# Performance work log

Measured on AMD Instinct MI355X. Metric: run time of the kernel, lower is better.

## Reference

```python
import jax, jax.numpy as jnp
import numpy as np

B, L, D, H, W = 2, 2048, 1024, 16, 32
HD = D // H  # head_dim = 64


def setup_inputs() -> dict:
    key = jax.random.key(0)
    ks = jax.random.split(key, 9)
    x = jax.random.normal(ks[0], (B, L, D), dtype=jnp.float32)
    s = 1.0 / np.sqrt(D)
    wq = jax.random.normal(ks[1], (D, D), dtype=jnp.float32) * s
    wk = jax.random.normal(ks[2], (D, D), dtype=jnp.float32) * s
    wv = jax.random.normal(ks[3], (D, D), dtype=jnp.float32) * s
    wo = jax.random.normal(ks[4], (D, D), dtype=jnp.float32) * s
    # per-head SwiGLU connection nets: in_dim=1, hidden=128, out_dim=1
    cw1 = jax.random.normal(ks[5], (H, 128), dtype=jnp.float32) * 0.5
    cw2 = jax.random.normal(ks[6], (H, 128), dtype=jnp.float32) * (1.0 / np.sqrt(128))
    cw3 = jax.random.normal(ks[7], (H, 128), dtype=jnp.float32) * 0.5
    # rotary embedding tables (complex freqs_cis -> cos/sin), [L, HD//2]
    inv_freq = 1.0 / (10000.0 ** (np.arange(0, HD, 2, dtype=np.float32) / HD))
    t = np.arange(L, dtype=np.float32)
    ang = np.outer(t, inv_freq)
    rope_cos = jnp.asarray(np.cos(ang), dtype=jnp.float32)
    rope_sin = jnp.asarray(np.sin(ang), dtype=jnp.float32)
    return {"x": x, "wq": wq, "wk": wk, "wv": wv, "wo": wo,
            "cw1": cw1, "cw2": cw2, "cw3": cw3,
            "rope_cos": rope_cos, "rope_sin": rope_sin,
            "window_size": W}


def _rope(t, cos, sin):
    # t: [B,H,L,HD]; cos/sin: [L,HD//2] -> broadcast [1,1,L,HD//2]
    tr = t.reshape(*t.shape[:-1], -1, 2)
    t0, t1 = tr[..., 0], tr[..., 1]
    c = cos[None, None]
    s = sin[None, None]
    r0 = t0 * c - t1 * s
    r1 = t0 * s + t1 * c
    return jnp.stack([r0, r1], axis=-1).reshape(t.shape)


def reference(x, wq, wk, wv, wo, cw1, cw2, cw3, rope_cos, rope_sin, window_size):
    b, l, d = x.shape
    h = cw1.shape[0]
    hd = d // h
    w = window_size
    # projections (torch Linear: y = x W^T)
    Q = jnp.einsum('bld,ed->ble', x, wq).reshape(b, l, h, hd).transpose(0, 2, 1, 3)
    K = jnp.einsum('bld,ed->ble', x, wk).reshape(b, l, h, hd).transpose(0, 2, 1, 3)
    V = jnp.einsum('bld,ed->ble', x, wv).reshape(b, l, h, hd).transpose(0, 2, 1, 3)
    Q = _rope(Q, rope_cos, rope_sin)
    K = _rope(K, rope_cos, rope_sin)
    # causal sliding windows via zero left-padding (matches torch F.pad + unfold;
    # NOTE: padded zeros are NOT masked in softmax, faithfully reproduced)
    pad = w - 1
    Kp = jnp.pad(K, ((0, 0), (0, 0), (pad, 0), (0, 0)))
    Vp = jnp.pad(V, ((0, 0), (0, 0), (pad, 0), (0, 0)))
    idx = jnp.arange(l)[:, None] + jnp.arange(w)[None, :]  # [L,W] into padded axis
    Kw = Kp[:, :, idx, :]  # [B,H,L,W,HD]
    Vw = Vp[:, :, idx, :]
    scores = jnp.einsum('bhld,bhlwd->bhlw', Q, Kw) / jnp.sqrt(jnp.float32(hd))
    attn = jax.nn.softmax(scores, axis=-1)
    # per-head learned position weights: SwiGLU(pos) for pos in linspace(0,1,W)
    pos = jnp.linspace(0.0, 1.0, w)  # [W]
    a1 = pos[None, :, None] * cw1[:, None, :]   # [H,W,128]
    a3 = pos[None, :, None] * cw3[:, None, :]
    conn = jnp.einsum('hwk,hk->hw', jax.nn.silu(a1) * a3, cw2)  # [H,W]
    conn = jax.nn.softmax(conn, axis=-1)
    final = attn * conn[None, :, None, :]
    final = final / (final.sum(axis=-1, keepdims=True) + 1e-9)
    out = jnp.einsum('bhlw,bhlwd->bhld', final, Vw)
    out = out.transpose(0, 2, 1, 3).reshape(b, l, d)
    return jnp.einsum('bld,ed->ble', out, wo)
```

## Files before the change

### kernel.cpp

```cpp
#include <hip/hip_runtime.h>
#include <math.h>

#define B 2
#define L 2048
#define D 1024
#define H 16
#define HD 64
#define W 32
#define M (B * L)
#define KP3 3072

typedef unsigned short ushort_t;
typedef short bf16x8 __attribute__((ext_vector_type(8)));
typedef float f32x4 __attribute__((ext_vector_type(4)));

static __device__ __forceinline__ unsigned short f2bf(float f) {
    union { float f; unsigned u; } v; v.f = f;
    unsigned r = v.u + 0x7FFF + ((v.u >> 16) & 1);
    return (unsigned short)(r >> 16);
}
static __device__ __forceinline__ float bf2f(unsigned short h) {
    union { unsigned u; float f; } v; v.u = ((unsigned)h) << 16;
    return v.f;
}
static __device__ __forceinline__ unsigned pk2(unsigned a, unsigned b) {
    return a | (b << 16);
}

__global__ __launch_bounds__(256) void pack_x_kernel(
    const float* __restrict__ src, ushort_t* __restrict__ dst)
{
    const int idx = blockIdx.x * 256 + threadIdx.x;
    const int r = idx >> 7;
    const int c = (idx & 127) << 3;
    const float* p = src + (size_t)r * D + c;
    const float4 f0 = *(const float4*)p;
    const float4 f1 = *(const float4*)(p + 4);
    float f[8] = {f0.x, f0.y, f0.z, f0.w, f1.x, f1.y, f1.z, f1.w};
    unsigned short h[8], lo[8];
#pragma unroll
    for (int i = 0; i < 8; ++i) {
        h[i] = f2bf(f[i]);
        lo[i] = f2bf(f[i] - bf2f(h[i]));
    }
    uint4 hv = make_uint4(pk2(h[0], h[1]), pk2(h[2], h[3]), pk2(h[4], h[5]), pk2(h[6], h[7]));
    uint4 lv = make_uint4(pk2(lo[0], lo[1]), pk2(lo[2], lo[3]), pk2(lo[4], lo[5]), pk2(lo[6], lo[7]));
    ushort_t* d = dst + (size_t)r * KP3 + c;
    *(uint4*)(d)         = hv;
    *(uint4*)(d + D)     = lv;
    *(uint4*)(d + 2 * D) = hv;
}

__global__ __launch_bounds__(256) void pack_w_kernel(
    const float* __restrict__ s0, const float* __restrict__ s1,
    const float* __restrict__ s2, ushort_t* __restrict__ dst, int nrows)
{
    const int idx = blockIdx.x * 256 + threadIdx.x;
    const int r = idx >> 7;
    if (r >= nrows) return;
    const int c = (idx & 127) << 3;
    const float* src = (r < 1024) ? s0 : ((r < 2048) ? s1 : s2);
    const float* p = src + (size_t)(r & 1023) * D + c;
    const float4 f0 = *(const float4*)p;
    const float4 f1 = *(const float4*)(p + 4);
    float f[8] = {f0.x, f0.y, f0.z, f0.w, f1.x, f1.y, f1.z, f1.w};
    unsigned short h[8], lo[8];
#pragma unroll
    for (int i = 0; i < 8; ++i) {
        h[i] = f2bf(f[i]);
        lo[i] = f2bf(f[i] - bf2f(h[i]));
    }
    uint4 hv = make_uint4(pk2(h[0], h[1]), pk2(h[2], h[3]), pk2(h[4], h[5]), pk2(h[6], h[7]));
    uint4 lv = make_uint4(pk2(lo[0], lo[1]), pk2(lo[2], lo[3]), pk2(lo[4], lo[5]), pk2(lo[6], lo[7]));
    ushort_t* d = dst + (size_t)r * KP3 + c;
    *(uint4*)(d)         = hv;
    *(uint4*)(d + D)     = hv;
    *(uint4*)(d + 2 * D) = lv;
}

__global__ __launch_bounds__(512) void conn_kernel(
    const float* __restrict__ cw1, const float* __restrict__ cw2,
    const float* __restrict__ cw3, float* __restrict__ conn)
{
    __shared__ float vals[H][W];
    const int t = threadIdx.x;
    const int h = t >> 5;
    const int w = t & 31;
    const float pos = (float)w / (float)(W - 1);
    float s = 0.f;
    for (int k = 0; k < 128; ++k) {
        const float a1 = pos * cw1[h * 128 + k];
        const float a3 = pos * cw3[h * 128 + k];
        const float si = a1 / (1.f + expf(-a1));
        s += si * a3 * cw2[h * 128 + k];
    }
    vals[h][w] = s;
    __syncthreads();
    float mx = -1e30f;
    for (int i = 0; i < W; ++i) mx = fmaxf(mx, vals[h][i]);
    float den = 0.f;
    for (int i = 0; i < W; ++i) den += expf(vals[h][i] - mx);
    conn[t] = expf(s - mx) / den;
}


#define SBAR() __builtin_amdgcn_s_barrier()
#define WAIT_LGKM0() { asm volatile("s_waitcnt lgkmcnt(0)" ::: "memory"); __builtin_amdgcn_sched_barrier(0); }
#define WAIT_VM(n)   { asm volatile("s_waitcnt vmcnt(" #n ")" ::: "memory"); __builtin_amdgcn_sched_barrier(0); }
#define PRIO1() __builtin_amdgcn_s_setprio(1)
#define PRIO0() __builtin_amdgcn_s_setprio(0)

#define STAGE_A(hh, tt, dd) do { \
    __builtin_amdgcn_global_load_lds((const __attribute__((address_space(1))) void*)(pA##hh##0 + (size_t)(tt) * 64), \
        (__attribute__((address_space(3))) void*)(lds + (dd) * 32768 + (hh) * 8192 + (w * 16 + 0) * 64), 16, 0, 0); \
    __builtin_amdgcn_global_load_lds((const __attribute__((address_space(1))) void*)(pA##hh##1 + (size_t)(tt) * 64), \
        (__attribute__((address_space(3))) void*)(lds + (dd) * 32768 + (hh) * 8192 + (w * 16 + 8) * 64), 16, 0, 0); \
} while (0)

#define STAGE_B(hh, tt, dd) do { \
    __builtin_amdgcn_global_load_lds((const __attribute__((address_space(1))) void*)(pB##hh##0 + (size_t)(tt) * 64), \
        (__attribute__((address_space(3))) void*)(lds + (dd) * 32768 + 16384 + (hh) * 8192 + (w * 16 + 0) * 64), 16, 0, 0); \
    __builtin_amdgcn_global_load_lds((const __attribute__((address_space(1))) void*)(pB##hh##1 + (size_t)(tt) * 64), \
        (__attribute__((address_space(3))) void*)(lds + (dd) * 32768 + 16384 + (hh) * 8192 + (w * 16 + 8) * 64), 16, 0, 0); \
} while (0)

#define READ_A(qm, dd) do { \
    _Pragma("unroll") for (int mi = 0; mi < 4; ++mi) { \
        a[mi][0] = *(const bf16x8*)(lds + (dd) * 32768 + (qm) * 8192 + (baseA + mi * 16) * 64 + ch0); \
        a[mi][1] = *(const bf16x8*)(lds + (dd) * 32768 + (qm) * 8192 + (baseA + mi * 16) * 64 + ch1); } \
} while (0)

#define READ_B(qn, dd, bb) do { \
    _Pragma("unroll") for (int ni = 0; ni < 2; ++ni) { \
        bb[ni][0] = *(const bf16x8*)(lds + (dd) * 32768 + 16384 + (qn) * 8192 + (baseB + ni * 16) * 64 + ch0); \
        bb[ni][1] = *(const bf16x8*)(lds + (dd) * 32768 + 16384 + (qn) * 8192 + (baseB + ni * 16) * 64 + ch1); } \
} while (0)

#define MMA(qm, qn, bb) do { \
    _Pragma("unroll") for (int mi = 0; mi < 4; ++mi) \
    _Pragma("unroll") for (int ni = 0; ni < 2; ++ni) { \
        acc[(qm)*4+mi][(qn)*2+ni] = __builtin_amdgcn_mfma_f32_16x16x32_bf16(a[mi][0], bb[ni][0], acc[(qm)*4+mi][(qn)*2+ni], 0, 0, 0); \
        acc[(qm)*4+mi][(qn)*2+ni] = __builtin_amdgcn_mfma_f32_16x16x32_bf16(a[mi][1], bb[ni][1], acc[(qm)*4+mi][(qn)*2+ni], 0, 0, 0); } \
} while (0)

__global__ __launch_bounds__(512, 2) void gemm8(
    const ushort_t* __restrict__ Ap, const ushort_t* __restrict__ Bp,
    int nkt, int mode, float* __restrict__ outp,
    float* __restrict__ qb, float* __restrict__ kb, float* __restrict__ vb,
    const float* __restrict__ rc, const float* __restrict__ rs)
{
    extern __shared__ short lds[];
    const int tid = threadIdx.x;
    const int w = tid >> 6;
    const int ln = tid & 63;
    const int wr = w >> 2, wc = w & 3;

    const int gx = gridDim.x;
    const int nwg = gx * gridDim.y;
    int fid = blockIdx.y * gx + blockIdx.x;
    fid = (fid & 7) * (nwg >> 3) + (fid >> 3);
    const int n0 = (fid % gx) * 256;
    const int m0 = (fid / gx) * 256;
    const int z = blockIdx.z;

    if (mode == 2) { Ap += (size_t)z * 1536; Bp += (size_t)z * 1536; }

    const int lchk = ((ln & 7) ^ (ln >> 3)) * 8;
    const ushort_t *pA00, *pA01, *pA10, *pA11, *pB00, *pB01, *pB10, *pB11;
    {
        const int r0 = w * 16 + (ln >> 3);
        const int r1 = w * 16 + 8 + (ln >> 3);
#define GROWA(rl, hh) (m0 + ((rl) & 63) + (((rl) >> 6) * 128) + (hh) * 64)
#define GROWB(rl, hh) (n0 + ((rl) & 31) + (((rl) >> 5) * 64) + (hh) * 32)
        pA00 = Ap + (size_t)GROWA(r0, 0) * KP3 + lchk;
        pA01 = Ap + (size_t)GROWA(r1, 0) * KP3 + lchk;
        pA10 = Ap + (size_t)GROWA(r0, 1) * KP3 + lchk;
        pA11 = Ap + (size_t)GROWA(r1, 1) * KP3 + lchk;
        pB00 = Bp + (size_t)GROWB(r0, 0) * KP3 + lchk;
        pB01 = Bp + (size_t)GROWB(r1, 0) * KP3 + lchk;
        pB10 = Bp + (size_t)GROWB(r0, 1) * KP3 + lchk;
        pB11 = Bp + (size_t)GROWB(r1, 1) * KP3 + lchk;
    }

    const int baseA = wr * 64 + (ln & 15);
    const int baseB = wc * 32 + (ln & 15);
    const int ch0 = ((0 * 4 + (ln >> 4)) ^ (ln & 7)) * 8;
    const int ch1 = ((1 * 4 + (ln >> 4)) ^ (ln & 7)) * 8;

    f32x4 acc[8][4];
#pragma unroll
    for (int i = 0; i < 8; ++i)
#pragma unroll
        for (int j = 0; j < 4; ++j) acc[i][j] = (f32x4){0.f, 0.f, 0.f, 0.f};

    bf16x8 a[4][2], b0[2][2], b1[2][2];

    STAGE_A(0, 0, 0); STAGE_B(0, 0, 0); STAGE_B(1, 0, 0); STAGE_A(1, 0, 0);
    STAGE_A(0, 1, 1); STAGE_B(0, 1, 1);
    WAIT_VM(8);
    SBAR();

    const int niters = nkt >> 1;
    for (int it = 0; it < niters; ++it) {
        const int t1 = 2 * it + 1;
        const int t2 = (2 * it + 2 < nkt) ? 2 * it + 2 : 0;
        const int t3 = (2 * it + 3 < nkt) ? 2 * it + 3 : 1;
        READ_A(0, 0); READ_B(0, 0, b0); STAGE_A(1, t1, 1);
        SBAR(); WAIT_LGKM0(); PRIO1(); MMA(0, 0, b0); PRIO0(); WAIT_VM(6); SBAR();
        READ_B(1, 0, b1); STAGE_B(1, t1, 1);
        SBAR(); WAIT_LGKM0(); PRIO1(); MMA(0, 1, b1); PRIO0(); SBAR();
        READ_A(1, 0); STAGE_A(0, t2, 0);
        SBAR(); WAIT_LGKM0(); PRIO1(); MMA(1, 0, b0); PRIO0(); SBAR();
        STAGE_B(0, t2, 0);
        SBAR(); PRIO1(); MMA(1, 1, b1); PRIO0(); WAIT_VM(8); SBAR();
        READ_A(0, 1); READ_B(0, 1, b0); STAGE_A(1, t2, 0);
        SBAR(); WAIT_LGKM0(); PRIO1(); MMA(0, 0, b0); PRIO0(); WAIT_VM(6); SBAR();
        READ_B(1, 1, b1); STAGE_B(1, t2, 0);
        SBAR(); WAIT_LGKM0(); PRIO1(); MMA(0, 1, b1); PRIO0(); SBAR();
        READ_A(1, 1); STAGE_A(0, t3, 1);
        SBAR(); WAIT_LGKM0(); PRIO1(); MMA(1, 0, b0); PRIO0(); SBAR();
        STAGE_B(0, t3, 1);
        SBAR(); PRIO1(); MMA(1, 1, b1); PRIO0(); WAIT_VM(8); SBAR();
    }

    if (mode == 1) {
#pragma unroll
        for (int mf = 0; mf < 8; ++mf)
#pragma unroll
            for (int nf = 0; nf < 4; ++nf)
#pragma unroll
                for (int j = 0; j < 4; ++j) {
                    const int m = m0 + wr * 128 + mf * 16 + (ln >> 4) * 4 + j;
                    const int n = n0 + wc * 64 + nf * 16 + (ln & 15);
                    const int which = n >> 10;
                    float* dst = (which == 0) ? qb : ((which == 1) ? kb : vb);
                    const int bb = m >> 11;
                    const int l = m & (L - 1);
                    const int nn = n & 1023;
                    const int hh = nn >> 6;
                    const int hd = nn & 63;
                    float v = acc[mf][nf][j];
                    if (which < 2) {
                        const int ip = hd >> 1;
                        const float c = rc[l * (HD / 2) + ip];
                        const float s = rs[l * (HD / 2) + ip];
                        const float p = __shfl_xor(v, 1);
                        v = (hd & 1) ? fmaf(p, s, v * c) : fmaf(p, -s, v * c);
                    }
                    dst[(((size_t)(bb * H + hh)) * L + l) * HD + hd] = v;
                }
    } else {
        float* dst = outp + (size_t)z * ((size_t)M * 1024);
#pragma unroll
        for (int mf = 0; mf < 8; ++mf)
#pragma unroll
            for (int nf = 0; nf < 4; ++nf)
#pragma unroll
                for (int j = 0; j < 4; ++j) {
                    const int m = m0 + wr * 128 + mf * 16 + (ln >> 4) * 4 + j;
                    const int n = n0 + wc * 64 + nf * 16 + (ln & 15);
                    dst[(size_t)m * 1024 + n] = acc[mf][nf][j];
                }
    }
}

__global__ __launch_bounds__(256) void reduce_kernel(
    const float* __restrict__ p, float* __restrict__ out)
{
    const size_t i = ((size_t)blockIdx.x * 256 + threadIdx.x) * 4;
    const float4 a = *(const float4*)(p + i);
    const float4 b = *(const float4*)(p + (size_t)M * 1024 + i);
    *(float4*)(out + i) = make_float4(a.x + b.x, a.y + b.y, a.z + b.z, a.w + b.w);
}

#define QT 64
#define KR (QT + W - 1)
#define KPAD 68

__global__ __launch_bounds__(256) void attn_kernel(
    const float* __restrict__ qb, const float* __restrict__ kb,
    const float* __restrict__ vb, const float* __restrict__ conn,
    float* __restrict__ ao)
{
    __shared__ float Ks[KR][KPAD];
    __shared__ float Vs[KR][KPAD];
    const int tid = threadIdx.x;
    const int r = tid >> 2;
    const int p = tid & 3;
    const int l0 = blockIdx.x * QT;
    const int bh = blockIdx.y;
    const int h = bh & (H - 1);
    const int bb = bh >> 4;
    const float* Qg = qb + (size_t)bh * L * HD;
    const float* Kg = kb + (size_t)bh * L * HD;
    const float* Vg = vb + (size_t)bh * L * HD;

    for (int idx = tid; idx < KR * 16; idx += 256) {
        const int rr = idx >> 4;
        const int f4 = (idx & 15) << 2;
        const int lr = l0 - (W - 1) + rr;
        float4 kv = make_float4(0, 0, 0, 0);
        float4 vv = make_float4(0, 0, 0, 0);
        if (lr >= 0) {
            kv = *(const float4*)(Kg + (size_t)lr * HD + f4);
            vv = *(const float4*)(Vg + (size_t)lr * HD + f4);
        }
        *(float4*)&Ks[rr][f4] = kv;
        *(float4*)&Vs[rr][f4] = vv;
    }

    const int l = l0 + r;
    float4 q[4];
#pragma unroll
    for (int i = 0; i < 4; ++i)
        q[i] = *(const float4*)(Qg + (size_t)l * HD + p * 16 + i * 4);

    __syncthreads();

    float sc[W];
#pragma unroll
    for (int w = 0; w < W; ++w) {
        const float* kr = &Ks[r + w][p * 16];
        float s = 0.f;
#pragma unroll
        for (int i = 0; i < 4; ++i) {
            const float4 kv = *(const float4*)(kr + i * 4);
            s = fmaf(q[i].x, kv.x, s);
            s = fmaf(q[i].y, kv.y, s);
            s = fmaf(q[i].z, kv.z, s);
            s = fmaf(q[i].w, kv.w, s);
        }
        s += __shfl_xor(s, 1);
        s += __shfl_xor(s, 2);
        sc[w] = s * 0.125f;
    }

    float mx = -1e30f;
#pragma unroll
    for (int w = 0; w < W; ++w) mx = fmaxf(mx, sc[w]);
    float den = 0.f;
#pragma unroll
    for (int w = 0; w < W; ++w) { sc[w] = expf(sc[w] - mx); den += sc[w]; }
    const float inv = 1.f / den;
    float fsum = 0.f;
#pragma unroll
    for (int w = 0; w < W; ++w) {
        sc[w] = sc[w] * inv * conn[h * W + w];
        fsum += sc[w];
    }
    const float rn = 1.f / (fsum + 1e-9f);

    float4 o[4];
#pragma unroll
    for (int i = 0; i < 4; ++i) o[i] = make_float4(0, 0, 0, 0);
#pragma unroll
    for (int w = 0; w < W; ++w) {
        const float wt = sc[w] * rn;
        const float* vr = &Vs[r + w][p * 16];
#pragma unroll
        for (int i = 0; i < 4; ++i) {
            const float4 vv = *(const float4*)(vr + i * 4);
            o[i].x = fmaf(wt, vv.x, o[i].x);
            o[i].y = fmaf(wt, vv.y, o[i].y);
            o[i].z = fmaf(wt, vv.z, o[i].z);
            o[i].w = fmaf(wt, vv.w, o[i].w);
        }
    }

    float* dst = ao + ((size_t)(bb * L + l) * D + h * HD + p * 16);
#pragma unroll
    for (int i = 0; i < 4; ++i) *(float4*)(dst + i * 4) = o[i];
}

extern "C" void kernel_launch(void* const* d_in, const int* in_sizes, int n_in,
                              void* d_out, int out_size, void* d_ws, size_t ws_size,
                              hipStream_t stream)
{
    const float* x   = (const float*)d_in[0];
    const float* wq  = (const float*)d_in[1];
    const float* wk  = (const float*)d_in[2];
    const float* wv  = (const float*)d_in[3];
    const float* wo  = (const float*)d_in[4];
    const float* cw1 = (const float*)d_in[5];
    const float* cw2 = (const float*)d_in[6];
    const float* cw3 = (const float*)d_in[7];
    const float* rc  = (const float*)d_in[8];
    const float* rs  = (const float*)d_in[9];
    float* out = (float*)d_out;

    float* ws = (float*)d_ws;
    float* conn = ws;
    float* qb = ws + 1024;
    float* kb = qb + (size_t)B * H * L * HD;
    float* vb = kb + (size_t)B * H * L * HD;
    ushort_t* xp    = (ushort_t*)(vb + (size_t)B * H * L * HD);
    ushort_t* wqkvp = xp + (size_t)M * KP3;
    ushort_t* wop   = wqkvp + (size_t)3072 * KP3;
    float* part = qb;
    float* ao = (float*)wqkvp;

    hipFuncSetAttribute((const void*)gemm8, hipFuncAttributeMaxDynamicSharedMemorySize, 131072);

    pack_x_kernel<<<dim3(M * 128 / 256), dim3(256), 0, stream>>>(x, xp);
    pack_w_kernel<<<dim3(3072 * 128 / 256), dim3(256), 0, stream>>>(wq, wk, wv, wqkvp, 3072);
    pack_w_kernel<<<dim3(1024 * 128 / 256), dim3(256), 0, stream>>>(wo, wo, wo, wop, 1024);
    conn_kernel<<<dim3(1), dim3(512), 0, stream>>>(cw1, cw2, cw3, conn);

    gemm8<<<dim3(12, 16, 1), dim3(512), 131072, stream>>>(
        xp, wqkvp, 48, 1, nullptr, qb, kb, vb, rc, rs);

    attn_kernel<<<dim3(L / QT, B * H), dim3(256), 0, stream>>>(qb, kb, vb, conn, ao);

    pack_x_kernel<<<dim3(M * 128 / 256), dim3(256), 0, stream>>>(ao, xp);

    gemm8<<<dim3(4, 16, 2), dim3(512), 131072, stream>>>(
        xp, wop, 24, 2, part, nullptr, nullptr, nullptr, rc, rs);

    reduce_kernel<<<dim3(M * 1024 / 1024), dim3(256), 0, stream>>>(part, out);
}
```

Before: 307.4 us.

## Double-buffer LDS fragment reads in GEMM and fuse attention output packing

The GEMM main loop now keeps separate A0/A1 register fragments and prefetches the next LDS fragments before each MFMA block. It uses partial lgkmcnt waits instead of full drains and drops the extra barriers, so LDS reads overlap with matrix math. The attention kernel writes its output directly in the split hi/lo bf16 packed layout, which removes the separate pack kernel and its fp32 round trip. The output projection switches from split-K 2 to split-K 3 with a three-way reduce, which adds more partial-sum traffic in exchange for more workgroups.

```diff
diff --git a/kernel.cpp b/kernel.cpp
--- a/kernel.cpp
+++ b/kernel.cpp
@@ -105,7 +105,7 @@
 
 
 #define SBAR() __builtin_amdgcn_s_barrier()
-#define WAIT_LGKM0() { asm volatile("s_waitcnt lgkmcnt(0)" ::: "memory"); __builtin_amdgcn_sched_barrier(0); }
+#define WAIT_LGKM(n) { asm volatile("s_waitcnt lgkmcnt(" #n ")" ::: "memory"); __builtin_amdgcn_sched_barrier(0); }
 #define WAIT_VM(n)   { asm volatile("s_waitcnt vmcnt(" #n ")" ::: "memory"); __builtin_amdgcn_sched_barrier(0); }
 #define PRIO1() __builtin_amdgcn_s_setprio(1)
 #define PRIO0() __builtin_amdgcn_s_setprio(0)
@@ -124,23 +124,32 @@
         (__attribute__((address_space(3))) void*)(lds + (dd) * 32768 + 16384 + (hh) * 8192 + (w * 16 + 8) * 64), 16, 0, 0); \
 } while (0)
 
-#define READ_A(qm, dd) do { \
+#define READ_A0(dd) do { \
     _Pragma("unroll") for (int mi = 0; mi < 4; ++mi) { \
-        a[mi][0] = *(const bf16x8*)(lds + (dd) * 32768 + (qm) * 8192 + (baseA + mi * 16) * 64 + ch0); \
-        a[mi][1] = *(const bf16x8*)(lds + (dd) * 32768 + (qm) * 8192 + (baseA + mi * 16) * 64 + ch1); } \
-} while (0)
-
-#define READ_B(qn, dd, bb) do { \
+        a0[mi][0] = *(const bf16x8*)(lds + (dd) * 32768 + (baseA + mi * 16) * 64 + ch0); \
+        a0[mi][1] = *(const bf16x8*)(lds + (dd) * 32768 + (baseA + mi * 16) * 64 + ch1); } \
+} while (0)
+#define READ_A1(dd) do { \
+    _Pragma("unroll") for (int mi = 0; mi < 4; ++mi) { \
+        a1[mi][0] = *(const bf16x8*)(lds + (dd) * 32768 + 8192 + (baseA + mi * 16) * 64 + ch0); \
+        a1[mi][1] = *(const bf16x8*)(lds + (dd) * 32768 + 8192 + (baseA + mi * 16) * 64 + ch1); } \
+} while (0)
+#define READ_B0(dd) do { \
     _Pragma("unroll") for (int ni = 0; ni < 2; ++ni) { \
-        bb[ni][0] = *(const bf16x8*)(lds + (dd) * 32768 + 16384 + (qn) * 8192 + (baseB + ni * 16) * 64 + ch0); \
-        bb[ni][1] = *(const bf16x8*)(lds + (dd) * 32768 + 16384 + (qn) * 8192 + (baseB + ni * 16) * 64 + ch1); } \
-} while (0)
-
-#define MMA(qm, qn, bb) do { \
+        b0[ni][0] = *(const bf16x8*)(lds + (dd) * 32768 + 16384 + (baseB + ni * 16) * 64 + ch0); \
+        b0[ni][1] = *(const bf16x8*)(lds + (dd) * 32768 + 16384 + (baseB + ni * 16) * 64 + ch1); } \
+} while (0)
+#define READ_B1(dd) do { \
+    _Pragma("unroll") for (int ni = 0; ni < 2; ++ni) { \
+        b1[ni][0] = *(const bf16x8*)(lds + (dd) * 32768 + 16384 + 8192 + (baseB + ni * 16) * 64 + ch0); \
+        b1[ni][1] = *(const bf16x8*)(lds + (dd) * 32768 + 16384 + 8192 + (baseB + ni * 16) * 64 + ch1); } \
+} while (0)
+
+#define MMA(qm, qn, aa, bb) do { \
     _Pragma("unroll") for (int mi = 0; mi < 4; ++mi) \
     _Pragma("unroll") for (int ni = 0; ni < 2; ++ni) { \
-        acc[(qm)*4+mi][(qn)*2+ni] = __builtin_amdgcn_mfma_f32_16x16x32_bf16(a[mi][0], bb[ni][0], acc[(qm)*4+mi][(qn)*2+ni], 0, 0, 0); \
-        acc[(qm)*4+mi][(qn)*2+ni] = __builtin_amdgcn_mfma_f32_16x16x32_bf16(a[mi][1], bb[ni][1], acc[(qm)*4+mi][(qn)*2+ni], 0, 0, 0); } \
+        acc[(qm)*4+mi][(qn)*2+ni] = __builtin_amdgcn_mfma_f32_16x16x32_bf16(aa[mi][0], bb[ni][0], acc[(qm)*4+mi][(qn)*2+ni], 0, 0, 0); \
+        acc[(qm)*4+mi][(qn)*2+ni] = __builtin_amdgcn_mfma_f32_16x16x32_bf16(aa[mi][1], bb[ni][1], acc[(qm)*4+mi][(qn)*2+ni], 0, 0, 0); } \
 } while (0)
 
 __global__ __launch_bounds__(512, 2) void gemm8(
@@ -163,7 +172,7 @@
     const int m0 = (fid / gx) * 256;
     const int z = blockIdx.z;
 
-    if (mode == 2) { Ap += (size_t)z * 1536; Bp += (size_t)z * 1536; }
+    if (mode == 2) { Ap += (size_t)z * 1024; Bp += (size_t)z * 1024; }
 
     const int lchk = ((ln & 7) ^ (ln >> 3)) * 8;
     const ushort_t *pA00, *pA01, *pA10, *pA11, *pB00, *pB01, *pB10, *pB11;
@@ -193,34 +202,35 @@
 #pragma unroll
         for (int j = 0; j < 4; ++j) acc[i][j] = (f32x4){0.f, 0.f, 0.f, 0.f};
 
-    bf16x8 a[4][2], b0[2][2], b1[2][2];
-
-    STAGE_A(0, 0, 0); STAGE_B(0, 0, 0); STAGE_B(1, 0, 0); STAGE_A(1, 0, 0);
+    bf16x8 a0[4][2], a1[4][2], b0[2][2], b1[2][2];
+
+    STAGE_A(0, 0, 0); STAGE_B(0, 0, 0); STAGE_A(1, 0, 0); STAGE_B(1, 0, 0);
     STAGE_A(0, 1, 1); STAGE_B(0, 1, 1);
-    WAIT_VM(8);
+    WAIT_VM(4);
     SBAR();
+    READ_A0(0); READ_B0(0);
 
     const int niters = nkt >> 1;
     for (int it = 0; it < niters; ++it) {
         const int t1 = 2 * it + 1;
         const int t2 = (2 * it + 2 < nkt) ? 2 * it + 2 : 0;
         const int t3 = (2 * it + 3 < nkt) ? 2 * it + 3 : 1;
-        READ_A(0, 0); READ_B(0, 0, b0); STAGE_A(1, t1, 1);
-        SBAR(); WAIT_LGKM0(); PRIO1(); MMA(0, 0, b0); PRIO0(); WAIT_VM(6); SBAR();
-        READ_B(1, 0, b1); STAGE_B(1, t1, 1);
-        SBAR(); WAIT_LGKM0(); PRIO1(); MMA(0, 1, b1); PRIO0(); SBAR();
-        READ_A(1, 0); STAGE_A(0, t2, 0);
-        SBAR(); WAIT_LGKM0(); PRIO1(); MMA(1, 0, b0); PRIO0(); SBAR();
-        STAGE_B(0, t2, 0);
-        SBAR(); PRIO1(); MMA(1, 1, b1); PRIO0(); WAIT_VM(8); SBAR();
-        READ_A(0, 1); READ_B(0, 1, b0); STAGE_A(1, t2, 0);
-        SBAR(); WAIT_LGKM0(); PRIO1(); MMA(0, 0, b0); PRIO0(); WAIT_VM(6); SBAR();
-        READ_B(1, 1, b1); STAGE_B(1, t2, 0);
-        SBAR(); WAIT_LGKM0(); PRIO1(); MMA(0, 1, b1); PRIO0(); SBAR();
-        READ_A(1, 1); STAGE_A(0, t3, 1);
-        SBAR(); WAIT_LGKM0(); PRIO1(); MMA(1, 0, b0); PRIO0(); SBAR();
-        STAGE_B(0, t3, 1);
-        SBAR(); PRIO1(); MMA(1, 1, b1); PRIO0(); WAIT_VM(8); SBAR();
+        READ_B1(0); STAGE_A(1, t1, 1);
+        WAIT_LGKM(4);  PRIO1(); MMA(0, 0, a0, b0); PRIO0(); WAIT_VM(6); SBAR();
+        READ_A1(0); STAGE_B(1, t1, 1);
+        WAIT_LGKM(8);  PRIO1(); MMA(0, 1, a0, b1); PRIO0(); WAIT_VM(6); SBAR();
+        READ_A0(1); STAGE_A(0, t2, 0);
+        WAIT_LGKM(8);  PRIO1(); MMA(1, 0, a1, b0); PRIO0(); WAIT_VM(6); SBAR();
+        READ_B0(1); STAGE_B(0, t2, 0);
+        WAIT_LGKM(12); PRIO1(); MMA(1, 1, a1, b1); PRIO0(); WAIT_VM(4); SBAR();
+        READ_B1(1); STAGE_A(1, t2, 0);
+        WAIT_LGKM(4);  PRIO1(); MMA(0, 0, a0, b0); PRIO0(); WAIT_VM(6); SBAR();
+        READ_A1(1); STAGE_B(1, t2, 0);
+        WAIT_LGKM(8);  PRIO1(); MMA(0, 1, a0, b1); PRIO0(); WAIT_VM(6); SBAR();
+        READ_A0(0); STAGE_A(0, t3, 1);
+        WAIT_LGKM(8);  PRIO1(); MMA(1, 0, a1, b0); PRIO0(); WAIT_VM(6); SBAR();
+        READ_B0(0); STAGE_B(0, t3, 1);
+        WAIT_LGKM(12); PRIO1(); MMA(1, 1, a1, b1); PRIO0(); WAIT_VM(4); SBAR();
     }
 
     if (mode == 1) {
@@ -270,7 +280,9 @@
     const size_t i = ((size_t)blockIdx.x * 256 + threadIdx.x) * 4;
     const float4 a = *(const float4*)(p + i);
     const float4 b = *(const float4*)(p + (size_t)M * 1024 + i);
-    *(float4*)(out + i) = make_float4(a.x + b.x, a.y + b.y, a.z + b.z, a.w + b.w);
+    const float4 c = *(const float4*)(p + (size_t)2 * M * 1024 + i);
+    *(float4*)(out + i) = make_float4(a.x + b.x + c.x, a.y + b.y + c.y,
+                                      a.z + b.z + c.z, a.w + b.w + c.w);
 }
 
 #define QT 64
@@ -280,7 +292,7 @@
 __global__ __launch_bounds__(256) void attn_kernel(
     const float* __restrict__ qb, const float* __restrict__ kb,
     const float* __restrict__ vb, const float* __restrict__ conn,
-    float* __restrict__ ao)
+    ushort_t* __restrict__ aop)
 {
     __shared__ float Ks[KR][KPAD];
     __shared__ float Vs[KR][KPAD];
@@ -367,9 +379,28 @@
         }
     }
 
-    float* dst = ao + ((size_t)(bb * L + l) * D + h * HD + p * 16);
-#pragma unroll
-    for (int i = 0; i < 4; ++i) *(float4*)(dst + i * 4) = o[i];
+    float f[16];
+#pragma unroll
+    for (int i = 0; i < 4; ++i) {
+        f[4 * i] = o[i].x; f[4 * i + 1] = o[i].y; f[4 * i + 2] = o[i].z; f[4 * i + 3] = o[i].w;
+    }
+    unsigned short hh16[16], lo16[16];
+#pragma unroll
+    for (int i = 0; i < 16; ++i) {
+        hh16[i] = f2bf(f[i]);
+        lo16[i] = f2bf(f[i] - bf2f(hh16[i]));
+    }
+    uint4 hv0 = make_uint4(pk2(hh16[0], hh16[1]), pk2(hh16[2], hh16[3]), pk2(hh16[4], hh16[5]), pk2(hh16[6], hh16[7]));
+    uint4 hv1 = make_uint4(pk2(hh16[8], hh16[9]), pk2(hh16[10], hh16[11]), pk2(hh16[12], hh16[13]), pk2(hh16[14], hh16[15]));
+    uint4 lv0 = make_uint4(pk2(lo16[0], lo16[1]), pk2(lo16[2], lo16[3]), pk2(lo16[4], lo16[5]), pk2(lo16[6], lo16[7]));
+    uint4 lv1 = make_uint4(pk2(lo16[8], lo16[9]), pk2(lo16[10], lo16[11]), pk2(lo16[12], lo16[13]), pk2(lo16[14], lo16[15]));
+    ushort_t* dp = aop + (size_t)(bb * L + l) * KP3 + h * HD + p * 16;
+    *(uint4*)(dp)             = hv0;
+    *(uint4*)(dp + 8)         = hv1;
+    *(uint4*)(dp + D)         = lv0;
+    *(uint4*)(dp + D + 8)     = lv1;
+    *(uint4*)(dp + 2 * D)     = hv0;
+    *(uint4*)(dp + 2 * D + 8) = hv1;
 }
 
 extern "C" void kernel_launch(void* const* d_in, const int* in_sizes, int n_in,
@@ -397,7 +428,6 @@
     ushort_t* wqkvp = xp + (size_t)M * KP3;
     ushort_t* wop   = wqkvp + (size_t)3072 * KP3;
     float* part = qb;
-    float* ao = (float*)wqkvp;
 
     hipFuncSetAttribute((const void*)gemm8, hipFuncAttributeMaxDynamicSharedMemorySize, 131072);
 
@@ -409,12 +439,10 @@
     gemm8<<<dim3(12, 16, 1), dim3(512), 131072, stream>>>(
         xp, wqkvp, 48, 1, nullptr, qb, kb, vb, rc, rs);
 
-    attn_kernel<<<dim3(L / QT, B * H), dim3(256), 0, stream>>>(qb, kb, vb, conn, ao);
-
-    pack_x_kernel<<<dim3(M * 128 / 256), dim3(256), 0, stream>>>(ao, xp);
-
-    gemm8<<<dim3(4, 16, 2), dim3(512), 131072, stream>>>(
-        xp, wop, 24, 2, part, nullptr, nullptr, nullptr, rc, rs);
+    attn_kernel<<<dim3(L / QT, B * H), dim3(256), 0, stream>>>(qb, kb, vb, conn, xp);
+
+    gemm8<<<dim3(4, 16, 3), dim3(512), 131072, stream>>>(
+        xp, wop, 16, 2, part, nullptr, nullptr, nullptr, rc, rs);
 
     reduce_kernel<<<dim3(M * 1024 / 1024), dim3(256), 0, stream>>>(part, out);
 }
```

Result: slower. 410.5 us (+33.5%).
